# Optimization experiments

Measured on AMD Instinct MI355X. Metric: run time of the kernel, lower is better.

The kernel has to match this reference:

```python
import jax, jax.numpy as jnp
import numpy as np

N_HEAD = 16
NEG = -1e10


def setup_inputs() -> dict:
    key = jax.random.key(0)
    ks = jax.random.split(key, 10)
    B, T, C = 2, 2048, 1024
    hs = C // N_HEAD
    inv = 1.0 / np.sqrt(C)
    return {
        "x": jax.random.normal(ks[0], (B, T, C), jnp.float32),
        "W1": jax.random.normal(ks[1], (C, C), jnp.float32) * inv,
        "bw1": jnp.zeros((C,), jnp.float32),
        "b1": jnp.zeros((hs,), jnp.float32),
        # original init: uniform(-0.001, 0.001)
        "w2": jax.random.uniform(ks[2], (hs, T), jnp.float32, -0.001, 0.001),
        "b2": jnp.zeros((T,), jnp.float32),
        "Wv": jax.random.normal(ks[3], (C, C), jnp.float32) * inv,
        "bv": jnp.zeros((C,), jnp.float32),
        "Wp": jax.random.normal(ks[4], (C, C), jnp.float32) * inv,
        "bp": jnp.zeros((C,), jnp.float32),
    }


def reference(x, W1, bw1, b1, w2, b2, Wv, bv, Wp, bp):
    B, T, C = x.shape
    nh = N_HEAD
    hs = C // nh
    # factorized synthesizer 'query': (B, nh, T, hs)
    h = (x @ W1 + bw1).reshape(B, T, nh, hs).transpose(0, 2, 1, 3)
    # scores: relu(h + b1) @ w2 + b2  -> (B, nh, T, T)
    att = jnp.einsum('bhtd,dk->bhtk', jax.nn.relu(h + b1), w2[:, :T]) + b2[:T]
    # causal mask then softmax (masked_fill with -1e10, as in original)
    causal = jnp.tril(jnp.ones((T, T), bool))
    att = jnp.where(causal[None, None], att, NEG)
    att = jax.nn.softmax(att, axis=-1)
    # values
    v = (x @ Wv + bv).reshape(B, T, nh, hs).transpose(0, 2, 1, 3)
    y = jnp.einsum('bhtk,bhkd->bhtd', att, v)
    y = y.transpose(0, 2, 1, 3).reshape(B, T, C)
    return y @ Wp + bp
```

## Files before the change

### kernel.cpp

```cpp
#include <hip/hip_runtime.h>
#include <hip/hip_bf16.h>

#define TSEQ 2048
#define CDIM 1024
#define NH 16
#define HS 64

typedef __attribute__((ext_vector_type(8))) short bf16x8;
typedef __attribute__((ext_vector_type(4))) float f32x4;
typedef __attribute__((ext_vector_type(16))) float f32x16;

__device__ inline void gload16(const void* g, void* l) {
    __builtin_amdgcn_global_load_lds((const __attribute__((address_space(1))) void*)g,
                                     (__attribute__((address_space(3))) void*)l, 16, 0, 0);
}
__device__ inline void gload4(const void* g, void* l) {
    __builtin_amdgcn_global_load_lds((const __attribute__((address_space(1))) void*)g,
                                     (__attribute__((address_space(3))) void*)l, 4, 0, 0);
}

__device__ inline unsigned packbf(float a, float b) {
    union { __hip_bfloat162 h; unsigned u; } cv;
    cv.h = __float22bfloat162_rn(make_float2(a, b));
    return cv.u;
}

__global__ __launch_bounds__(256)
void conv_bf16(const float* __restrict__ in, __hip_bfloat16* __restrict__ out, int n) {
    int i = (blockIdx.x * 256 + threadIdx.x) * 4;
    if (i + 3 < n) {
        float4 v = *(const float4*)(in + i);
        union { ushort4 u; __hip_bfloat16 h[4]; } o;
        o.h[0] = __float2bfloat16(v.x);
        o.h[1] = __float2bfloat16(v.y);
        o.h[2] = __float2bfloat16(v.z);
        o.h[3] = __float2bfloat16(v.w);
        *(ushort4*)((unsigned short*)out + i) = o.u;
    }
}

__global__ __launch_bounds__(256)
void b2_log2e(const float* __restrict__ b2, float* __restrict__ bl, int n) {
    int i = blockIdx.x * 256 + threadIdx.x;
    if (i < n) bl[i] = b2[i] * 1.44269504f;
}

__global__ __launch_bounds__(256)
void transpose_to_bf16(const float* __restrict__ in, __hip_bfloat16* __restrict__ out,
                       int R, int C) {
    __shared__ float t[32][33];
    const int tx = threadIdx.x & 31, ty = threadIdx.x >> 5;
    const int r0 = blockIdx.y * 32, c0 = blockIdx.x * 32;
    #pragma unroll
    for (int i = 0; i < 32; i += 8)
        t[ty + i][tx] = in[(size_t)(r0 + ty + i) * C + c0 + tx];
    __syncthreads();
    #pragma unroll
    for (int i = 0; i < 32; i += 8)
        out[(size_t)(c0 + ty + i) * R + r0 + tx] = __float2bfloat16(t[tx][ty + i]);
}

__global__ __launch_bounds__(256)
void transpose3_to_bf16(const float* __restrict__ W1, const float* __restrict__ Wv,
                        const float* __restrict__ Wp, __hip_bfloat16* __restrict__ o1,
                        __hip_bfloat16* __restrict__ o2, __hip_bfloat16* __restrict__ o3) {
    __shared__ float t[32][33];
    const float* in = blockIdx.z == 0 ? W1 : (blockIdx.z == 1 ? Wv : Wp);
    __hip_bfloat16* out = blockIdx.z == 0 ? o1 : (blockIdx.z == 1 ? o2 : o3);
    const int tx = threadIdx.x & 31, ty = threadIdx.x >> 5;
    const int r0 = blockIdx.y * 32, c0 = blockIdx.x * 32;
    #pragma unroll
    for (int i = 0; i < 32; i += 8)
        t[ty + i][tx] = in[(size_t)(r0 + ty + i) * CDIM + c0 + tx];
    __syncthreads();
    #pragma unroll
    for (int i = 0; i < 32; i += 8)
        out[(size_t)(c0 + ty + i) * CDIM + r0 + tx] = __float2bfloat16(t[tx][ty + i]);
}

__global__ __launch_bounds__(256, 2)
void gemm_qv(const __hip_bfloat16* __restrict__ X, const __hip_bfloat16* __restrict__ W,
             const float* __restrict__ bw1, const float* __restrict__ b1,
             const float* __restrict__ bv, __hip_bfloat16* __restrict__ Hb,
             __hip_bfloat16* __restrict__ Vblk, int M)
{
    __shared__ __align__(16) __hip_bfloat16 As[128 * 32];
    __shared__ __align__(16) __hip_bfloat16 Bs[128 * 32];
    const int tid = threadIdx.x, wave = tid >> 6, lane = tid & 63;
    const int wr = wave >> 1, wc = wave & 1, l15 = lane & 15, l4 = lane >> 4;
    const int m0 = blockIdx.y * 128, n0 = blockIdx.x * 128;
    const int K = CDIM;
    const int Bb = M >> 11;
    const int srow = wave * 32 + (lane >> 2), scol = (lane & 3) * 8;
    const __hip_bfloat16* xg = X + (size_t)(m0 + srow) * K + scol;
    const __hip_bfloat16* wg = W + (size_t)(n0 + srow) * K + scol;
    __hip_bfloat16* la = &As[wave * 32 * 32];
    __hip_bfloat16* lb = &Bs[wave * 32 * 32];

    f32x4 acc[4][4] = {};
    for (int k0 = 0; k0 < K; k0 += 32) {
        __syncthreads();
        gload16(xg + k0, la);
        gload16(xg + k0 + (size_t)16 * K, la + 16 * 32);
        gload16(wg + k0, lb);
        gload16(wg + k0 + (size_t)16 * K, lb + 16 * 32);
        __syncthreads();
        bf16x8 af[4], bfr[4];
        #pragma unroll
        for (int f = 0; f < 4; f++) af[f]  = *(const bf16x8*)&As[(wr * 64 + f * 16 + l15) * 32 + l4 * 8];
        #pragma unroll
        for (int f = 0; f < 4; f++) bfr[f] = *(const bf16x8*)&Bs[(wc * 64 + f * 16 + l15) * 32 + l4 * 8];
        #pragma unroll
        for (int fr = 0; fr < 4; fr++)
            #pragma unroll
            for (int fc = 0; fc < 4; fc++)
                acc[fr][fc] = __builtin_amdgcn_mfma_f32_16x16x32_bf16(af[fr], bfr[fc], acc[fr][fc], 0, 0, 0);
    }

    const bool isH = (n0 < CDIM);
    const int sl4 = ((l4 & 1) << 1) | (l4 >> 1);
    if (isH) {
        #pragma unroll
        for (int fc = 0; fc < 4; fc++) {
            const int col = n0 + wc * 64 + fc * 16 + l15;
            const float bias = bw1[col] + b1[col & (HS - 1)];
            #pragma unroll
            for (int fr = 0; fr < 4; fr++)
                #pragma unroll
                for (int r = 0; r < 4; r++) {
                    const int row = m0 + wr * 64 + fr * 16 + l4 * 4 + r;
                    const float hv = fmaxf(acc[fr][fc][r] + bias, 0.f) * 1.44269504f;
                    Hb[(size_t)row * CDIM + col] = __float2bfloat16(hv);
                }
        }
    } else {
        const int mt = m0 + wr * 64;
        const int bb = mt >> 11;
        const int ktb = (mt & (TSEQ - 1)) >> 6;
        const int hh = ((n0 - CDIM) + wc * 64) >> 6;
        __hip_bfloat16* tile = Vblk + (((size_t)hh * Bb + bb) * (TSEQ / 64) + ktb) * (HS * 64);
        #pragma unroll
        for (int fc = 0; fc < 4; fc++) {
            const int d = fc * 16 + l15;
            const int c2 = hh * HS + d;
            const float bias = bv[c2];
            #pragma unroll
            for (int fr = 0; fr < 4; fr++) {
                const int tl = fr * 16 + sl4 * 4;
                union { ushort4 u; __hip_bfloat16 h[4]; } o;
                #pragma unroll
                for (int r = 0; r < 4; r++) o.h[r] = __float2bfloat16(acc[fr][fc][r] + bias);
                *(ushort4*)(tile + (size_t)d * 64 + tl) = o.u;
            }
        }
    }
}

__global__ __launch_bounds__(256, 2)
void gemm_proj(const __hip_bfloat16* __restrict__ X, const __hip_bfloat16* __restrict__ Wt,
               const float* __restrict__ bN, float* __restrict__ Out, int M)
{
    __shared__ __align__(16) __hip_bfloat16 As[128 * 32];
    __shared__ __align__(16) __hip_bfloat16 Bs[128 * 32];
    const int tid = threadIdx.x, wave = tid >> 6, lane = tid & 63;
    const int wr = wave >> 1, wc = wave & 1, l15 = lane & 15, l4 = lane >> 4;
    const int m0 = blockIdx.y * 128, n0 = blockIdx.x * 128;
    const int K = CDIM;
    const int srow = wave * 32 + (lane >> 2), scol = (lane & 3) * 8;
    const __hip_bfloat16* xg = X + (size_t)(m0 + srow) * K + scol;
    const __hip_bfloat16* wg = Wt + (size_t)(n0 + srow) * K + scol;
    __hip_bfloat16* la = &As[wave * 32 * 32];
    __hip_bfloat16* lb = &Bs[wave * 32 * 32];

    f32x4 acc[4][4] = {};
    for (int k0 = 0; k0 < K; k0 += 32) {
        __syncthreads();
        gload16(xg + k0, la);
        gload16(xg + k0 + (size_t)16 * K, la + 16 * 32);
        gload16(wg + k0, lb);
        gload16(wg + k0 + (size_t)16 * K, lb + 16 * 32);
        __syncthreads();
        bf16x8 af[4], bfr[4];
        #pragma unroll
        for (int f = 0; f < 4; f++) af[f]  = *(const bf16x8*)&As[(wr * 64 + f * 16 + l15) * 32 + l4 * 8];
        #pragma unroll
        for (int f = 0; f < 4; f++) bfr[f] = *(const bf16x8*)&Bs[(wc * 64 + f * 16 + l15) * 32 + l4 * 8];
        #pragma unroll
        for (int fr = 0; fr < 4; fr++)
            #pragma unroll
            for (int fc = 0; fc < 4; fc++)
                acc[fr][fc] = __builtin_amdgcn_mfma_f32_16x16x32_bf16(af[fr], bfr[fc], acc[fr][fc], 0, 0, 0);
    }

    #pragma unroll
    for (int fc = 0; fc < 4; fc++) {
        const int col = n0 + wc * 64 + fc * 16 + l15;
        const float bias = bN[col];
        #pragma unroll
        for (int fr = 0; fr < 4; fr++)
            #pragma unroll
            for (int r = 0; r < 4; r++) {
                const int row = m0 + wr * 64 + fr * 16 + l4 * 4 + r;
                Out[(size_t)row * CDIM + col] = acc[fr][fc][r] + bias;
            }
    }
}

#define STAGEKV(KT, BUF) do {                                                   \
    gload16(kg0 + (size_t)(KT) * (64 * HS), &Ks[BUF][(w * 16) * 64]);           \
    gload16(kg1 + (size_t)(KT) * (64 * HS), &Ks[BUF][(w * 16 + 8) * 64]);       \
    gload16(vg0 + (size_t)(KT) * (HS * 64), &Vs[BUF][(w * 16) * 64]);           \
    gload16(vg1 + (size_t)(KT) * (HS * 64), &Vs[BUF][(w * 16 + 8) * 64]);       \
    if (w == 0) gload4(blg + (size_t)(KT) * 64, &blr[BUF][0]);                  \
} while (0)

__global__ __launch_bounds__(256, 2)
void attn_mfma14(const __hip_bfloat16* __restrict__ H, const __hip_bfloat16* __restrict__ w2t,
                 const __hip_bfloat16* __restrict__ Vblk, const float* __restrict__ bl,
                 __hip_bfloat16* __restrict__ Y, int M)
{
    __shared__ __align__(16) __hip_bfloat16 Ks[3][64 * 64];
    __shared__ __align__(16) __hip_bfloat16 Vs[3][64 * 64];
    __shared__ __align__(16) float blr[3][64];
    __shared__ float Ls[4 * 32];

    const int tid = threadIdx.x;
    const int w = tid >> 6, lane = tid & 63;
    const int l31 = lane & 31, hi = lane >> 5;
    const int h = blockIdx.y, b = blockIdx.z;
    const int u = (blockIdx.x + blockIdx.y) & 15;
    const int qb = b ? (15 - u) : u;
    const int q0 = qb * 128;
    const int qw = q0 + w * 32;
    const int swz = l31 & 7;
    const int Bb = M >> 11;

    const int srr = lane >> 3, spc = lane & 7;
    const int sr0 = w * 16 + srr, sr1 = sr0 + 8;
    const int sc = (spc ^ srr) * 8;
    const __hip_bfloat16* kg0 = w2t + (size_t)sr0 * HS + sc;
    const __hip_bfloat16* kg1 = w2t + (size_t)sr1 * HS + sc;
    const __hip_bfloat16* vpan = Vblk + (((size_t)h * Bb + b) * (TSEQ / 64)) * (HS * 64);
    const __hip_bfloat16* vg0 = vpan + (size_t)sr0 * 64 + sc;
    const __hip_bfloat16* vg1 = vpan + (size_t)sr1 * 64 + sc;
    const float* blg = bl + lane;

    bf16x8 hf[4];
    {
        const size_t row = (size_t)(b * TSEQ + qw + l31);
        #pragma unroll
        for (int kk = 0; kk < 4; kk++)
            hf[kk] = *(const bf16x8*)(H + row * CDIM + h * HS + kk * 16 + hi * 8);
    }

    f32x16 yacc[2] = {};
    float lsum = 0.f;
    const int ntile = 2 * qb + 2;

    STAGEKV(0, 0);
    STAGEKV(1, 1);

    for (int kt = 0; kt < ntile; kt++) {
        const int k0 = kt * 64;
        if (kt + 1 < ntile) asm volatile("s_waitcnt vmcnt(5)" ::: "memory");
        else                asm volatile("s_waitcnt vmcnt(0)" ::: "memory");
        __builtin_amdgcn_s_barrier();
        __builtin_amdgcn_sched_barrier(0);
        if (kt + 2 < ntile) STAGEKV(kt + 2, (kt + 2) % 3);
        if (k0 <= qw + 31) {
            const int buf = kt % 3;
            const bool nomask = (k0 + 63 <= qw);
            bf16x8 pa[4];
            #pragma unroll
            for (int tf = 0; tf < 2; tf++) {
                f32x16 st;
                #pragma unroll
                for (int g = 0; g < 4; g++) {
                    float4 blv = *(const float4*)&blr[buf][tf * 32 + g * 8 + hi * 4];
                    st[g * 4 + 0] = blv.x; st[g * 4 + 1] = blv.y;
                    st[g * 4 + 2] = blv.z; st[g * 4 + 3] = blv.w;
                }
                #pragma unroll
                for (int kk = 0; kk < 4; kk++) {
                    const int cs = (kk * 2 + hi) ^ swz;
                    bf16x8 kf = *(const bf16x8*)((const char*)&Ks[buf][0] + (tf * 32 + l31) * 128 + cs * 16);
                    st = __builtin_amdgcn_mfma_f32_32x32x16_bf16(kf, hf[kk], st, 0, 0, 0);
                }
                const int qg = qw + l31;
                float p[16];
                #pragma unroll
                for (int r = 0; r < 16; r++) {
                    float e = __builtin_amdgcn_exp2f(st[r]);
                    if (!nomask) {
                        const int tg = k0 + tf * 32 + (r & 3) + 8 * (r >> 2) + 4 * hi;
                        if (tg > qg) e = 0.f;
                    }
                    p[r] = e;
                    lsum += e;
                }
                #pragma unroll
                for (int m = 0; m < 2; m++) {
                    union { unsigned d[4]; bf16x8 v; } pk;
                    #pragma unroll
                    for (int dw = 0; dw < 4; dw++)
                        pk.d[dw] = packbf(p[8 * m + 2 * dw], p[8 * m + 2 * dw + 1]);
                    pa[tf * 2 + m] = pk.v;
                }
            }
            #pragma unroll
            for (int ks = 0; ks < 4; ks++) {
                const int cs = (ks * 2 + hi) ^ swz;
                #pragma unroll
                for (int df = 0; df < 2; df++) {
                    bf16x8 vf = *(const bf16x8*)((const char*)&Vs[buf][0] + (df * 32 + l31) * 128 + cs * 16);
                    yacc[df] = __builtin_amdgcn_mfma_f32_32x32x16_bf16(pa[ks], vf, yacc[df], 0, 0, 0);
                }
            }
        }
    }
    __syncthreads();

    lsum += __shfl_xor(lsum, 32);
    if (hi == 0) Ls[w * 32 + l31] = lsum;
    __syncthreads();

    #pragma unroll
    for (int g = 0; g < 4; g++) {
        float4 lv = *(const float4*)&Ls[w * 32 + g * 8 + hi * 4];
        #pragma unroll
        for (int df = 0; df < 2; df++)
            #pragma unroll
            for (int rr = 0; rr < 4; rr++) {
                const float v = yacc[df][g * 4 + rr] / ((const float*)&lv)[rr];
                const size_t row = (size_t)(b * TSEQ + qw + 8 * g + 4 * hi + rr);
                Y[row * CDIM + h * HS + df * 32 + l31] = __float2bfloat16(v);
            }
    }
}

extern "C" void kernel_launch(void* const* d_in, const int* in_sizes, int n_in,
                              void* d_out, int out_size, void* d_ws, size_t ws_size,
                              hipStream_t stream) {
    const float* x   = (const float*)d_in[0];
    const float* W1  = (const float*)d_in[1];
    const float* bw1 = (const float*)d_in[2];
    const float* b1  = (const float*)d_in[3];
    const float* w2  = (const float*)d_in[4];
    const float* b2  = (const float*)d_in[5];
    const float* Wv  = (const float*)d_in[6];
    const float* bv  = (const float*)d_in[7];
    const float* Wp  = (const float*)d_in[8];
    const float* bp  = (const float*)d_in[9];
    float* out = (float*)d_out;

    const int B = in_sizes[0] / (TSEQ * CDIM);
    const int M = B * TSEQ;
    const size_t MC = (size_t)M * CDIM;
    const size_t WC = (size_t)CDIM * CDIM;

    __hip_bfloat16* xb  = (__hip_bfloat16*)d_ws;
    __hip_bfloat16* Wqv = xb  + MC;
    __hip_bfloat16* Wpt = Wqv + 2 * WC;
    __hip_bfloat16* w2t = Wpt + WC;
    __hip_bfloat16* Hb  = w2t + (size_t)TSEQ * HS;
    __hip_bfloat16* Vbk = Hb  + MC;
    __hip_bfloat16* Yb  = Vbk + MC;
    float*          bl  = (float*)(Yb + MC);

    dim3 blk(256);
    conv_bf16<<<dim3((unsigned)(MC / 1024)), blk, 0, stream>>>(x, xb, (int)MC);
    b2_log2e<<<dim3(TSEQ / 256), blk, 0, stream>>>(b2, bl, TSEQ);
    transpose3_to_bf16<<<dim3(32, 32, 3), blk, 0, stream>>>(W1, Wv, Wp, Wqv, Wqv + WC, Wpt);
    transpose_to_bf16<<<dim3(TSEQ / 32, HS / 32), blk, 0, stream>>>(w2, w2t, HS, TSEQ);

    gemm_qv<<<dim3(16, M / 128), blk, 0, stream>>>(xb, Wqv, bw1, b1, bv, Hb, Vbk, M);

    attn_mfma14<<<dim3(16, NH, B), blk, 0, stream>>>(Hb, w2t, Vbk, bl, Yb, M);

    gemm_proj<<<dim3(8, M / 128), blk, 0, stream>>>(Yb, Wpt, bp, out, M);
}
```

Before: 123.1 us.

## Split attention key tiles across two wave halves with paired query tiles

New measurement: 126.8 us. +3.0%, slower.

```diff
diff --git a/kernel.cpp b/kernel.cpp
--- a/kernel.cpp
+++ b/kernel.cpp
@@ -207,42 +207,43 @@
 }
 
 #define STAGEKV(KT, BUF) do {                                                   \
-    gload16(kg0 + (size_t)(KT) * (64 * HS), &Ks[BUF][(w * 16) * 64]);           \
-    gload16(kg1 + (size_t)(KT) * (64 * HS), &Ks[BUF][(w * 16 + 8) * 64]);       \
-    gload16(vg0 + (size_t)(KT) * (HS * 64), &Vs[BUF][(w * 16) * 64]);           \
-    gload16(vg1 + (size_t)(KT) * (HS * 64), &Vs[BUF][(w * 16 + 8) * 64]);       \
-    if (w == 0) gload4(blg + (size_t)(KT) * 64, &blr[BUF][0]);                  \
+    gload16(kg + (size_t)(KT) * (64 * HS), KsP + (BUF) * 4096 + (w * 8) * 64);  \
+    gload16(vg + (size_t)(KT) * (HS * 64), VsP + (BUF) * 4096 + (w * 8) * 64);  \
+    gload4(blg + (size_t)(KT) * 64, &blr[BUF][0]);                              \
 } while (0)
 
-__global__ __launch_bounds__(256, 2)
-void attn_mfma14(const __hip_bfloat16* __restrict__ H, const __hip_bfloat16* __restrict__ w2t,
+__global__ __launch_bounds__(512, 2)
+void attn_mfma15(const __hip_bfloat16* __restrict__ H, const __hip_bfloat16* __restrict__ w2t,
                  const __hip_bfloat16* __restrict__ Vblk, const float* __restrict__ bl,
                  __hip_bfloat16* __restrict__ Y, int M)
 {
-    __shared__ __align__(16) __hip_bfloat16 Ks[3][64 * 64];
-    __shared__ __align__(16) __hip_bfloat16 Vs[3][64 * 64];
+    __shared__ __align__(16) char smem[49152];
     __shared__ __align__(16) float blr[3][64];
-    __shared__ float Ls[4 * 32];
+    __shared__ float LSL[4][64];
+    __shared__ float Lfin[4 * 32];
+    __hip_bfloat16* KsP = (__hip_bfloat16*)smem;
+    __hip_bfloat16* VsP = (__hip_bfloat16*)(smem + 24576);
 
     const int tid = threadIdx.x;
     const int w = tid >> 6, lane = tid & 63;
     const int l31 = lane & 31, hi = lane >> 5;
-    const int h = blockIdx.y, b = blockIdx.z;
-    const int u = (blockIdx.x + blockIdx.y) & 15;
-    const int qb = b ? (15 - u) : u;
-    const int q0 = qb * 128;
-    const int qw = q0 + w * 32;
+    const int hb = blockIdx.x;
+    const int h = hb & 15, b = hb >> 4;
+    const int ps = (blockIdx.y + blockIdx.x) & 15;
+    const int pi = ps >> 1, sg = ps & 1;
+    const int half = w >> 2, wl = w & 3;
+    const int qsel = wl >> 1, subl = wl & 1;
+    const int qtile = qsel ? (15 - pi) : pi;
+    const int qw = qtile * 128 + (sg * 2 + subl) * 32;
     const int swz = l31 & 7;
     const int Bb = M >> 11;
 
     const int srr = lane >> 3, spc = lane & 7;
-    const int sr0 = w * 16 + srr, sr1 = sr0 + 8;
+    const int sr = w * 8 + srr;
     const int sc = (spc ^ srr) * 8;
-    const __hip_bfloat16* kg0 = w2t + (size_t)sr0 * HS + sc;
-    const __hip_bfloat16* kg1 = w2t + (size_t)sr1 * HS + sc;
+    const __hip_bfloat16* kg = w2t + (size_t)sr * HS + sc;
     const __hip_bfloat16* vpan = Vblk + (((size_t)h * Bb + b) * (TSEQ / 64)) * (HS * 64);
-    const __hip_bfloat16* vg0 = vpan + (size_t)sr0 * 64 + sc;
-    const __hip_bfloat16* vg1 = vpan + (size_t)sr1 * 64 + sc;
+    const __hip_bfloat16* vg = vpan + (size_t)sr * 64 + sc;
     const float* blg = bl + lane;
 
     bf16x8 hf[4];
@@ -255,19 +256,20 @@
 
     f32x16 yacc[2] = {};
     float lsum = 0.f;
-    const int ntile = 2 * qb + 2;
+    const int lastkt = (qw + 31) >> 6;
+    const int ntile = (((15 - pi) * 128 + (sg * 2 + 1) * 32 + 31) >> 6) + 1;
 
     STAGEKV(0, 0);
     STAGEKV(1, 1);
 
     for (int kt = 0; kt < ntile; kt++) {
         const int k0 = kt * 64;
-        if (kt + 1 < ntile) asm volatile("s_waitcnt vmcnt(5)" ::: "memory");
+        if (kt + 1 < ntile) asm volatile("s_waitcnt vmcnt(3)" ::: "memory");
         else                asm volatile("s_waitcnt vmcnt(0)" ::: "memory");
         __builtin_amdgcn_s_barrier();
         __builtin_amdgcn_sched_barrier(0);
         if (kt + 2 < ntile) STAGEKV(kt + 2, (kt + 2) % 3);
-        if (k0 <= qw + 31) {
+        if (((kt ^ half) & 1) == 0 && kt <= lastkt) {
             const int buf = kt % 3;
             const bool nomask = (k0 + 63 <= qw);
             bf16x8 pa[4];
@@ -283,7 +285,7 @@
                 #pragma unroll
                 for (int kk = 0; kk < 4; kk++) {
                     const int cs = (kk * 2 + hi) ^ swz;
-                    bf16x8 kf = *(const bf16x8*)((const char*)&Ks[buf][0] + (tf * 32 + l31) * 128 + cs * 16);
+                    bf16x8 kf = *(const bf16x8*)((const char*)KsP + buf * 8192 + (tf * 32 + l31) * 128 + cs * 16);
                     st = __builtin_amdgcn_mfma_f32_32x32x16_bf16(kf, hf[kk], st, 0, 0, 0);
                 }
                 const int qg = qw + l31;
@@ -312,7 +314,7 @@
                 const int cs = (ks * 2 + hi) ^ swz;
                 #pragma unroll
                 for (int df = 0; df < 2; df++) {
-                    bf16x8 vf = *(const bf16x8*)((const char*)&Vs[buf][0] + (df * 32 + l31) * 128 + cs * 16);
+                    bf16x8 vf = *(const bf16x8*)((const char*)VsP + buf * 8192 + (df * 32 + l31) * 128 + cs * 16);
                     yacc[df] = __builtin_amdgcn_mfma_f32_32x32x16_bf16(pa[ks], vf, yacc[df], 0, 0, 0);
                 }
             }
@@ -320,21 +322,48 @@
     }
     __syncthreads();
 
-    lsum += __shfl_xor(lsum, 32);
-    if (hi == 0) Ls[w * 32 + l31] = lsum;
+    float4* LSY = (float4*)smem;
+    if (half == 1) {
+        #pragma unroll
+        for (int df = 0; df < 2; df++)
+            #pragma unroll
+            for (int g = 0; g < 4; g++) {
+                float4 t;
+                t.x = yacc[df][g * 4 + 0]; t.y = yacc[df][g * 4 + 1];
+                t.z = yacc[df][g * 4 + 2]; t.w = yacc[df][g * 4 + 3];
+                LSY[((wl * 2 + df) * 4 + g) * 64 + lane] = t;
+            }
+        LSL[wl][lane] = lsum;
+    }
     __syncthreads();
-
-    #pragma unroll
-    for (int g = 0; g < 4; g++) {
-        float4 lv = *(const float4*)&Ls[w * 32 + g * 8 + hi * 4];
+    if (half == 0) {
+        lsum += LSL[wl][lane];
         #pragma unroll
         for (int df = 0; df < 2; df++)
             #pragma unroll
-            for (int rr = 0; rr < 4; rr++) {
-                const float v = yacc[df][g * 4 + rr] / ((const float*)&lv)[rr];
-                const size_t row = (size_t)(b * TSEQ + qw + 8 * g + 4 * hi + rr);
-                Y[row * CDIM + h * HS + df * 32 + l31] = __float2bfloat16(v);
-            }
+            for (int g = 0; g < 4; g++) {
+                float4 t = LSY[((wl * 2 + df) * 4 + g) * 64 + lane];
+                yacc[df][g * 4 + 0] += t.x; yacc[df][g * 4 + 1] += t.y;
+                yacc[df][g * 4 + 2] += t.z; yacc[df][g * 4 + 3] += t.w;
+            }
+        lsum += __shfl_xor(lsum, 32);
+        if (hi == 0) Lfin[wl * 32 + l31] = lsum;
+    }
+    __syncthreads();
+
+    if (half == 0) {
+        #pragma unroll
+        for (int g = 0; g < 4; g++) {
+            float4 lv = *(const float4*)&Lfin[wl * 32 + g * 8 + hi * 4];
+            #pragma unroll
+            for (int df = 0; df < 2; df++)
+                #pragma unroll
+                for (int rr = 0; rr < 4; rr++) {
+                    const float v = yacc[df][g * 4 + rr] / ((const float*)&lv)[rr];
+                    const size_t row = (size_t)(b * TSEQ + qw + 8 * g + 4 * hi + rr);
+                    Y[row * CDIM + h * HS + df * 32 + l31] = __float2bfloat16(v);
+                }
+        }
     }
 }
 
@@ -375,7 +404,7 @@
 
     gemm_qv<<<dim3(16, M / 128), blk, 0, stream>>>(xb, Wqv, bw1, b1, bv, Hb, Vbk, M);
 
-    attn_mfma14<<<dim3(16, NH, B), blk, 0, stream>>>(Hb, w2t, Vbk, bl, Yb, M);
+    attn_mfma15<<<dim3(16 * B, 16), dim3(512), 0, stream>>>(Hb, w2t, Vbk, bl, Yb, M);
 
     gemm_proj<<<dim3(8, M / 128), blk, 0, stream>>>(Yb, Wpt, bp, out, M);
 }
```

## Pair complementary causal query tiles in 512-thread attention blocks sharing K/V staging

Applied to the files above, without the earlier changes.

After: 136.6 us. 1.11x slower.

```diff
diff --git a/kernel.cpp b/kernel.cpp
--- a/kernel.cpp
+++ b/kernel.cpp
@@ -207,42 +207,37 @@
 }
 
 #define STAGEKV(KT, BUF) do {                                                   \
-    gload16(kg0 + (size_t)(KT) * (64 * HS), &Ks[BUF][(w * 16) * 64]);           \
-    gload16(kg1 + (size_t)(KT) * (64 * HS), &Ks[BUF][(w * 16 + 8) * 64]);       \
-    gload16(vg0 + (size_t)(KT) * (HS * 64), &Vs[BUF][(w * 16) * 64]);           \
-    gload16(vg1 + (size_t)(KT) * (HS * 64), &Vs[BUF][(w * 16 + 8) * 64]);       \
-    if (w == 0) gload4(blg + (size_t)(KT) * 64, &blr[BUF][0]);                  \
+    gload16(kg + (size_t)(KT) * (64 * HS), &Ks[BUF][(w * 8) * 64]);             \
+    gload16(vg + (size_t)(KT) * (HS * 64), &Vs[BUF][(w * 8) * 64]);             \
+    gload4(blg + (size_t)(KT) * 64, &blr[BUF][0]);                              \
 } while (0)
 
-__global__ __launch_bounds__(256, 2)
-void attn_mfma14(const __hip_bfloat16* __restrict__ H, const __hip_bfloat16* __restrict__ w2t,
+__global__ __launch_bounds__(512, 1)
+void attn_mfma19(const __hip_bfloat16* __restrict__ H, const __hip_bfloat16* __restrict__ w2t,
                  const __hip_bfloat16* __restrict__ Vblk, const float* __restrict__ bl,
                  __hip_bfloat16* __restrict__ Y, int M)
 {
     __shared__ __align__(16) __hip_bfloat16 Ks[3][64 * 64];
     __shared__ __align__(16) __hip_bfloat16 Vs[3][64 * 64];
     __shared__ __align__(16) float blr[3][64];
-    __shared__ float Ls[4 * 32];
+    __shared__ float Ls[8 * 32];
 
     const int tid = threadIdx.x;
     const int w = tid >> 6, lane = tid & 63;
     const int l31 = lane & 31, hi = lane >> 5;
+    const int pr = blockIdx.x;
     const int h = blockIdx.y, b = blockIdx.z;
-    const int u = (blockIdx.x + blockIdx.y) & 15;
-    const int qb = b ? (15 - u) : u;
-    const int q0 = qb * 128;
-    const int qw = q0 + w * 32;
+    const int qtile = (w & 1) ? (15 - pr) : pr;
+    const int qw = qtile * 128 + (w >> 1) * 32;
     const int swz = l31 & 7;
     const int Bb = M >> 11;
 
     const int srr = lane >> 3, spc = lane & 7;
-    const int sr0 = w * 16 + srr, sr1 = sr0 + 8;
+    const int sr = w * 8 + srr;
     const int sc = (spc ^ srr) * 8;
-    const __hip_bfloat16* kg0 = w2t + (size_t)sr0 * HS + sc;
-    const __hip_bfloat16* kg1 = w2t + (size_t)sr1 * HS + sc;
+    const __hip_bfloat16* kg = w2t + (size_t)sr * HS + sc;
     const __hip_bfloat16* vpan = Vblk + (((size_t)h * Bb + b) * (TSEQ / 64)) * (HS * 64);
-    const __hip_bfloat16* vg0 = vpan + (size_t)sr0 * 64 + sc;
-    const __hip_bfloat16* vg1 = vpan + (size_t)sr1 * 64 + sc;
+    const __hip_bfloat16* vg = vpan + (size_t)sr * 64 + sc;
     const float* blg = bl + lane;
 
     bf16x8 hf[4];
@@ -255,19 +250,20 @@
 
     f32x16 yacc[2] = {};
     float lsum = 0.f;
-    const int ntile = 2 * qb + 2;
+    const int lastkt = (qw + 31) >> 6;
+    const int ntile = 2 * (15 - pr) + 2;
 
     STAGEKV(0, 0);
     STAGEKV(1, 1);
 
     for (int kt = 0; kt < ntile; kt++) {
         const int k0 = kt * 64;
-        if (kt + 1 < ntile) asm volatile("s_waitcnt vmcnt(5)" ::: "memory");
+        if (kt + 1 < ntile) asm volatile("s_waitcnt vmcnt(3)" ::: "memory");
         else                asm volatile("s_waitcnt vmcnt(0)" ::: "memory");
         __builtin_amdgcn_s_barrier();
         __builtin_amdgcn_sched_barrier(0);
         if (kt + 2 < ntile) STAGEKV(kt + 2, (kt + 2) % 3);
-        if (k0 <= qw + 31) {
+        if (kt <= lastkt) {
             const int buf = kt % 3;
             const bool nomask = (k0 + 63 <= qw);
             bf16x8 pa[4];
@@ -375,7 +371,7 @@
 
     gemm_qv<<<dim3(16, M / 128), blk, 0, stream>>>(xb, Wqv, bw1, b1, bv, Hb, Vbk, M);
 
-    attn_mfma14<<<dim3(16, NH, B), blk, 0, stream>>>(Hb, w2t, Vbk, bl, Yb, M);
+    attn_mfma19<<<dim3(8, NH, B), dim3(512), 0, stream>>>(Hb, w2t, Vbk, bl, Yb, M);
 
     gemm_proj<<<dim3(8, M / 128), blk, 0, stream>>>(Yb, Wpt, bp, out, M);
 }
```
